# Kernel optimization log

Hardware: AMD Instinct MI355X
Metric: run time of the kernel (lower is better)

Reference implementation:

```python
import jax, jax.numpy as jnp
import numpy as np

B, H, S, D = 2, 16, 2048, 128


def _make_omask(n_heads, seqlen, dtype=jnp.float32):
    # RetNet decay mask: omask[0, h, i, j] = gamma_h^(i-j) for i >= j, else 0
    gamma = 1.0 - 2.0 ** (-5.0 - jnp.arange(n_heads, dtype=jnp.float32))  # [H]
    i = jnp.arange(seqlen)[:, None]
    j = jnp.arange(seqlen)[None, :]
    tri = i >= j                                            # [S, S] lower-triangular incl. diag
    expo = jnp.where(tri, (i - j).astype(jnp.float32), 0.0)  # clamp exponent to avoid overflow
    mask = jnp.where(tri[None], gamma[:, None, None] ** expo[None], 0.0)  # [H, S, S]
    return mask[None].astype(dtype)                          # [1, H, S, S]


def setup_inputs() -> dict:
    key = jax.random.key(0)
    kq, kk, kv = jax.random.split(key, 3)
    q = jax.random.normal(kq, (B, H, S, D), dtype=jnp.float32)
    k = jax.random.normal(kk, (B, H, S, D), dtype=jnp.float32)
    v = jax.random.normal(kv, (B, H, S, D), dtype=jnp.float32)
    omask = _make_omask(H, S)
    return {"q": q, "k": k, "v": v, "omask": omask}


def reference(q, k, v, omask):
    mask = omask[0]                                   # [H, S, S]
    L = jnp.sum(omask, axis=-1, keepdims=True)        # [1, H, S, 1] row sums of decay mask
    qL = q / L                                        # [B, H, S, D]
    # decay-masked retention scores: ((q/L) @ k^T) * D
    scores = jnp.einsum('bhid,bhjd->bhij', qL, k) * mask[None]  # [B, H, S, S]
    # P[b,h,i] = sum_j scores = qL . (mask @ k)  (== einsum with Tbf in original)
    P = jnp.clip(jnp.abs(jnp.sum(scores, axis=-1)), 1.0, None)[..., None]  # [B,H,S,1]
    P = jax.lax.stop_gradient(P)                      # original uses .detach()
    O = jnp.einsum('bhij,bhjd->bhid', scores, v) / P  # [B, H, S, D]
    return O
```

## Files before the change

### kernel.cpp

```cpp
#include <hip/hip_runtime.h>
#include <hip/hip_bf16.h>

namespace {

constexpr int S_DIM = 2048;
constexpr int D_DIM = 128;
constexpr int NH    = 16;
constexpr int QBLK  = 128;
constexpr int KJ    = 32;
constexpr int KROWB = 272;

typedef float  f32x16 __attribute__((ext_vector_type(16)));
typedef __bf16 bf16x8 __attribute__((ext_vector_type(8)));

union U4 { unsigned int w[4]; bf16x8 v; };

__device__ __forceinline__ unsigned int pk2(float a, float b) {
  union { __bf16 h[2]; unsigned int u; } x;
  x.h[0] = (__bf16)a; x.h[1] = (__bf16)b;
  return x.u;
}

__global__ __launch_bounds__(256, 2)
void retnet_fwd(const float* __restrict__ qg, const float* __restrict__ kg,
                const float* __restrict__ vg, float* __restrict__ og) {
  __shared__ __align__(16) unsigned char kbuf[2][KJ * KROWB];

  const int tid  = threadIdx.x;
  const int wave = tid >> 6;
  const int lane = tid & 63;
  const int l31  = lane & 31;
  const int hi   = lane >> 5;

  const int bh = blockIdx.x;
  const int y  = blockIdx.y;
  const int qtile = (y < 8) ? y : (23 - y);
  const int h  = bh & (NH - 1);
  const int qb = qtile * QBLK;

  const float u    = exp2f(-(float)(5 + h));
  const float lng  = log1pf(-u);
  const float lg2g = lng * 1.44269504088896340736f;

  const long long base = (long long)bh * S_DIM * D_DIM;
  const float* qp = qg + base;
  const float* kp = kg + base;
  const float* vp = vg + base;
  float*       op = og + base;

  const int wrow0 = qb + 32 * wave;
  const int ig    = wrow0 + l31;
  const float qscale = -u / expm1f((float)(ig + 1) * lng);

  bf16x8 qf[8];
  {
    const float* qrow = qp + (long long)ig * D_DIM;
    #pragma unroll
    for (int kk = 0; kk < 8; ++kk) {
      const int d0 = 16 * kk + 8 * hi;
      float4 a = *(const float4*)(qrow + d0);
      float4 b = *(const float4*)(qrow + d0 + 4);
      U4 t;
      t.w[0] = pk2(a.x * qscale, a.y * qscale);
      t.w[1] = pk2(a.z * qscale, a.w * qscale);
      t.w[2] = pk2(b.x * qscale, b.y * qscale);
      t.w[3] = pk2(b.z * qscale, b.w * qscale);
      qf[kk] = t.v;
    }
  }

  const float gi1 = exp2f(-lg2g);
  const float gi8 = exp2f(-8.0f * lg2g);
  const float g4[4] = {1.0f, gi1, gi1 * gi1, gi1 * gi1 * gi1};
  const float g8[4] = {1.0f, gi8, gi8 * gi8, gi8 * gi8 * gi8};
  const float gih = hi ? exp2f(-4.0f * lg2g) : 1.0f;

  f32x16 oacc[4] = {};
  float rowsum = 0.0f;

  const int NT     = 4 * qtile + 4;
  const int twlast = 4 * qtile + wave;

  const int sj = tid >> 3;
  const int sd = (tid & 7) * 16;

  float4 ka[4];
  auto loadK = [&](int t) {
    const float* kr = kp + (long long)(KJ * t + sj) * D_DIM + sd;
    #pragma unroll
    for (int c = 0; c < 4; ++c) ka[c] = *(const float4*)(kr + 4 * c);
  };

  auto storeK = [&](int buf) {
    const int s0 = sd >> 3;
    unsigned char* kb = kbuf[buf] + sj * KROWB;
    U4 t;
    t.w[0] = pk2(ka[0].x, ka[0].y); t.w[1] = pk2(ka[0].z, ka[0].w);
    t.w[2] = pk2(ka[1].x, ka[1].y); t.w[3] = pk2(ka[1].z, ka[1].w);
    *(bf16x8*)(kb + (((s0    ) ^ (sj & 15)) * 16)) = t.v;
    t.w[0] = pk2(ka[2].x, ka[2].y); t.w[1] = pk2(ka[2].z, ka[2].w);
    t.w[2] = pk2(ka[3].x, ka[3].y); t.w[3] = pk2(ka[3].z, ka[3].w);
    *(bf16x8*)(kb + (((s0 + 1) ^ (sj & 15)) * 16)) = t.v;
  };

  loadK(0);
  storeK(0);
  __syncthreads();

  for (int t = 0; t < NT; ++t) {
    const int cur = t & 1;
    const bool pre = (t + 1 < NT);
    if (pre) loadK(t + 1);
    __builtin_amdgcn_sched_barrier(0);

    if (t <= twlast) {
      const unsigned char* kb = kbuf[cur];

      f32x16 acc = {};
      #pragma unroll
      for (int kk = 0; kk < 8; ++kk) {
        bf16x8 kf = *(const bf16x8*)(kb + l31 * KROWB + (((2 * kk + hi) ^ (l31 & 15)) * 16));
        acc = __builtin_amdgcn_mfma_f32_32x32x16_bf16(kf, qf[kk], acc, 0, 0, 0);
      }

      const float bb = exp2f((float)(ig - KJ * t) * lg2g) * gih;
      float sv[16];
      if (t == twlast) {
        #pragma unroll
        for (int r = 0; r < 16; ++r) {
          const int jl = (r & 3) + 8 * (r >> 2) + 4 * hi;
          float s = acc[r] * (bb * g8[r >> 2] * g4[r & 3]);
          s = (l31 >= jl) ? s : 0.0f;
          rowsum += s; sv[r] = s;
        }
      } else {
        #pragma unroll
        for (int r = 0; r < 16; ++r) {
          const float s = acc[r] * (bb * g8[r >> 2] * g4[r & 3]);
          rowsum += s; sv[r] = s;
        }
      }

      unsigned int W[4][2], XW[4][2];
      #pragma unroll
      for (int qd = 0; qd < 4; ++qd) {
        W[qd][0] = pk2(sv[4 * qd + 0], sv[4 * qd + 1]);
        W[qd][1] = pk2(sv[4 * qd + 2], sv[4 * qd + 3]);
      }
      #pragma unroll
      for (int qd = 0; qd < 4; ++qd) {
        XW[qd][0] = (unsigned int)__shfl_xor((int)W[qd][0], 32, 64);
        XW[qd][1] = (unsigned int)__shfl_xor((int)W[qd][1], 32, 64);
      }

      #pragma unroll
      for (int jc = 0; jc < 2; ++jc) {
        U4 af;
        if (hi == 0) {
          af.w[0] = W[2 * jc][0];      af.w[1] = W[2 * jc][1];
          af.w[2] = XW[2 * jc][0];     af.w[3] = XW[2 * jc][1];
        } else {
          af.w[0] = XW[2 * jc + 1][0]; af.w[1] = XW[2 * jc + 1][1];
          af.w[2] = W[2 * jc + 1][0];  af.w[3] = W[2 * jc + 1][1];
        }
        const float* vbase =
            vp + (long long)(KJ * t + 16 * jc + 8 * hi) * D_DIM + l31;
        #pragma unroll
        for (int dc = 0; dc < 4; ++dc) {
          const float* vcol = vbase + 32 * dc;
          float ve[8];
          #pragma unroll
          for (int e = 0; e < 8; ++e) ve[e] = vcol[e * D_DIM];
          U4 vf;
          vf.w[0] = pk2(ve[0], ve[1]); vf.w[1] = pk2(ve[2], ve[3]);
          vf.w[2] = pk2(ve[4], ve[5]); vf.w[3] = pk2(ve[6], ve[7]);
          oacc[dc] = __builtin_amdgcn_mfma_f32_32x32x16_bf16(af.v, vf.v, oacc[dc], 0, 0, 0);
        }
      }
    }

    if (pre) storeK(cur ^ 1);
    __syncthreads();
  }

  const float tot  = rowsum + __shfl_xor(rowsum, 32, 64);
  const float invp = 1.0f / fmaxf(fabsf(tot), 1.0f);

  #pragma unroll
  for (int r = 0; r < 16; ++r) {
    const int il = (r & 3) + 8 * (r >> 2) + 4 * hi;
    const float pr = __shfl(invp, il, 32);
    float* orow = op + (long long)(wrow0 + il) * D_DIM + l31;
    #pragma unroll
    for (int dc = 0; dc < 4; ++dc)
      orow[32 * dc] = oacc[dc][r] * pr;
  }
}

}

extern "C" void kernel_launch(void* const* d_in, const int* in_sizes, int n_in,
                              void* d_out, int out_size, void* d_ws, size_t ws_size,
                              hipStream_t stream) {
  const float* q = (const float*)d_in[0];
  const float* k = (const float*)d_in[1];
  const float* v = (const float*)d_in[2];
  float* o = (float*)d_out;
  dim3 grid(32 , 16);
  retnet_fwd<<<grid, 256, 0, stream>>>(q, k, v, o);
}
```

Measured before the change: 506.2 us.

## Precast K to bf16 and transpose V in workspace, split KV across two waves

Two pre-pass kernels convert K to bf16 and write a bf16 transposed copy of V into the workspace. The main kernel then loads its MFMA operands straight from global memory, with no LDS staging, no block-wide syncs and no per-element strided V gathers. The grid is reorganised so each block of two waves owns one 32-row query tile. The waves split the key tiles between them by parity and combine partial outputs and row sums through LDS at the end. This removes repeated fp32-to-bf16 conversion and the uncoalesced V reads, at the cost of extra launches and an extra round trip through workspace memory.

```diff
diff --git a/kernel.cpp b/kernel.cpp
--- a/kernel.cpp
+++ b/kernel.cpp
@@ -6,9 +6,8 @@
 constexpr int S_DIM = 2048;
 constexpr int D_DIM = 128;
 constexpr int NH    = 16;
-constexpr int QBLK  = 128;
-constexpr int KJ    = 32;
-constexpr int KROWB = 272;
+constexpr long long KV_ELEMS = 32LL * S_DIM * D_DIM;
+constexpr size_t    WS_NEED  = (size_t)(2 * KV_ELEMS) * 2;
 
 typedef float  f32x16 __attribute__((ext_vector_type(16)));
 typedef __bf16 bf16x8 __attribute__((ext_vector_type(8)));
@@ -21,10 +20,54 @@
   return x.u;
 }
 
-__global__ __launch_bounds__(256, 2)
-void retnet_fwd(const float* __restrict__ qg, const float* __restrict__ kg,
-                const float* __restrict__ vg, float* __restrict__ og) {
-  __shared__ __align__(16) unsigned char kbuf[2][KJ * KROWB];
+__global__ __launch_bounds__(256)
+void conv_k(const float* __restrict__ k, unsigned short* __restrict__ kw) {
+  const long long i = 8LL * (blockIdx.x * 256 + threadIdx.x);
+  float4 a = *(const float4*)(k + i);
+  float4 b = *(const float4*)(k + i + 4);
+  U4 t;
+  t.w[0] = pk2(a.x, a.y); t.w[1] = pk2(a.z, a.w);
+  t.w[2] = pk2(b.x, b.y); t.w[3] = pk2(b.z, b.w);
+  *(bf16x8*)(kw + i) = t.v;
+}
+
+__global__ __launch_bounds__(256)
+void transp_v(const float* __restrict__ v, unsigned short* __restrict__ vt) {
+  __shared__ float lds[32][33];
+  const int bid = blockIdx.x;
+  const int bh  = bid >> 8;
+  const int rem = bid & 255;
+  const int j0  = (rem >> 2) * 32;
+  const int d0  = (rem & 3) * 32;
+  const int tid = threadIdx.x;
+
+  {
+    const int jl = tid >> 3;
+    const int d4 = (tid & 7) * 4;
+    float4 x = *(const float4*)(v + ((long long)bh * S_DIM + j0 + jl) * D_DIM + d0 + d4);
+    lds[d4 + 0][jl] = x.x; lds[d4 + 1][jl] = x.y;
+    lds[d4 + 2][jl] = x.z; lds[d4 + 3][jl] = x.w;
+  }
+  __syncthreads();
+  {
+    const int dl = tid >> 3;
+    const int j4 = (tid & 7) * 4;
+    const unsigned int w0 = pk2(lds[dl][j4 + 0], lds[dl][j4 + 1]);
+    const unsigned int w1 = pk2(lds[dl][j4 + 2], lds[dl][j4 + 3]);
+    const unsigned long long w = (unsigned long long)w0 | ((unsigned long long)w1 << 32);
+    *(unsigned long long*)(vt + ((long long)bh * D_DIM + d0 + dl) * S_DIM + j0 + j4) = w;
+  }
+}
+
+template <bool PRE>
+__global__ __launch_bounds__(128, 3)
+void retnet_main(const float* __restrict__ qg, const float* __restrict__ kg,
+                 const float* __restrict__ vg,
+                 const unsigned short* __restrict__ kw,
+                 const unsigned short* __restrict__ vtw,
+                 float* __restrict__ og) {
+  __shared__ float xbuf[2][2][64][20];
+  __shared__ float rsbuf[2][32];
 
   const int tid  = threadIdx.x;
   const int wave = tid >> 6;
@@ -32,11 +75,10 @@
   const int l31  = lane & 31;
   const int hi   = lane >> 5;
 
-  const int bh = blockIdx.x;
-  const int y  = blockIdx.y;
-  const int qtile = (y < 8) ? y : (23 - y);
-  const int h  = bh & (NH - 1);
-  const int qb = qtile * QBLK;
+  const int bid = blockIdx.x;
+  const int g   = 63 - (bid >> 5);
+  const int bh  = bid & 31;
+  const int h   = bh & (NH - 1);
 
   const float u    = exp2f(-(float)(5 + h));
   const float lng  = log1pf(-u);
@@ -48,7 +90,7 @@
   const float* vp = vg + base;
   float*       op = og + base;
 
-  const int wrow0 = qb + 32 * wave;
+  const int wrow0 = 32 * g;
   const int ig    = wrow0 + l31;
   const float qscale = -u / expm1f((float)(ig + 1) * lng);
 
@@ -78,93 +120,82 @@
   f32x16 oacc[4] = {};
   float rowsum = 0.0f;
 
-  const int NT     = 4 * qtile + 4;
-  const int twlast = 4 * qtile + wave;
-
-  const int sj = tid >> 3;
-  const int sd = (tid & 7) * 16;
-
-  float4 ka[4];
-  auto loadK = [&](int t) {
-    const float* kr = kp + (long long)(KJ * t + sj) * D_DIM + sd;
-    #pragma unroll
-    for (int c = 0; c < 4; ++c) ka[c] = *(const float4*)(kr + 4 * c);
-  };
-
-  auto storeK = [&](int buf) {
-    const int s0 = sd >> 3;
-    unsigned char* kb = kbuf[buf] + sj * KROWB;
-    U4 t;
-    t.w[0] = pk2(ka[0].x, ka[0].y); t.w[1] = pk2(ka[0].z, ka[0].w);
-    t.w[2] = pk2(ka[1].x, ka[1].y); t.w[3] = pk2(ka[1].z, ka[1].w);
-    *(bf16x8*)(kb + (((s0    ) ^ (sj & 15)) * 16)) = t.v;
-    t.w[0] = pk2(ka[2].x, ka[2].y); t.w[1] = pk2(ka[2].z, ka[2].w);
-    t.w[2] = pk2(ka[3].x, ka[3].y); t.w[3] = pk2(ka[3].z, ka[3].w);
-    *(bf16x8*)(kb + (((s0 + 1) ^ (sj & 15)) * 16)) = t.v;
-  };
-
-  loadK(0);
-  storeK(0);
-  __syncthreads();
-
-  for (int t = 0; t < NT; ++t) {
-    const int cur = t & 1;
-    const bool pre = (t + 1 < NT);
-    if (pre) loadK(t + 1);
-    __builtin_amdgcn_sched_barrier(0);
-
-    if (t <= twlast) {
-      const unsigned char* kb = kbuf[cur];
-
-      f32x16 acc = {};
+  const unsigned short* kwb = kw  + (long long)bh * S_DIM * D_DIM;
+  const unsigned short* vtb = vtw + (long long)bh * D_DIM * S_DIM;
+
+  for (int t = wave; t <= g; t += 2) {
+    const int j0 = 32 * t;
+
+    f32x16 acc = {};
+    if (PRE) {
+      const unsigned short* kb = kwb + (long long)(j0 + l31) * D_DIM + 8 * hi;
       #pragma unroll
       for (int kk = 0; kk < 8; ++kk) {
-        bf16x8 kf = *(const bf16x8*)(kb + l31 * KROWB + (((2 * kk + hi) ^ (l31 & 15)) * 16));
+        bf16x8 kf = *(const bf16x8*)(kb + 16 * kk);
         acc = __builtin_amdgcn_mfma_f32_32x32x16_bf16(kf, qf[kk], acc, 0, 0, 0);
       }
-
-      const float bb = exp2f((float)(ig - KJ * t) * lg2g) * gih;
-      float sv[16];
-      if (t == twlast) {
+    } else {
+      const float* kr = kp + (long long)(j0 + l31) * D_DIM + 8 * hi;
+      #pragma unroll
+      for (int kk = 0; kk < 8; ++kk) {
+        float4 a = *(const float4*)(kr + 16 * kk);
+        float4 b = *(const float4*)(kr + 16 * kk + 4);
+        U4 t;
+        t.w[0] = pk2(a.x, a.y); t.w[1] = pk2(a.z, a.w);
+        t.w[2] = pk2(b.x, b.y); t.w[3] = pk2(b.z, b.w);
+        acc = __builtin_amdgcn_mfma_f32_32x32x16_bf16(t.v, qf[kk], acc, 0, 0, 0);
+      }
+    }
+
+    const float bb = exp2f((float)(ig - j0) * lg2g) * gih;
+    float sv[16];
+    if (t == g) {
+      #pragma unroll
+      for (int r = 0; r < 16; ++r) {
+        const int jl = (r & 3) + 8 * (r >> 2) + 4 * hi;
+        float s = acc[r] * (bb * g8[r >> 2] * g4[r & 3]);
+        s = (l31 >= jl) ? s : 0.0f;
+        rowsum += s; sv[r] = s;
+      }
+    } else {
+      #pragma unroll
+      for (int r = 0; r < 16; ++r) {
+        const float s = acc[r] * (bb * g8[r >> 2] * g4[r & 3]);
+        rowsum += s; sv[r] = s;
+      }
+    }
+
+    unsigned int W[4][2], XW[4][2];
+    #pragma unroll
+    for (int qd = 0; qd < 4; ++qd) {
+      W[qd][0] = pk2(sv[4 * qd + 0], sv[4 * qd + 1]);
+      W[qd][1] = pk2(sv[4 * qd + 2], sv[4 * qd + 3]);
+    }
+    #pragma unroll
+    for (int qd = 0; qd < 4; ++qd) {
+      XW[qd][0] = (unsigned int)__shfl_xor((int)W[qd][0], 32, 64);
+      XW[qd][1] = (unsigned int)__shfl_xor((int)W[qd][1], 32, 64);
+    }
+
+    #pragma unroll
+    for (int jc = 0; jc < 2; ++jc) {
+      U4 af;
+      if (hi == 0) {
+        af.w[0] = W[2 * jc][0];      af.w[1] = W[2 * jc][1];
+        af.w[2] = XW[2 * jc][0];     af.w[3] = XW[2 * jc][1];
+      } else {
+        af.w[0] = XW[2 * jc + 1][0]; af.w[1] = XW[2 * jc + 1][1];
+        af.w[2] = W[2 * jc + 1][0];  af.w[3] = W[2 * jc + 1][1];
+      }
+      if (PRE) {
+        const unsigned short* vrow = vtb + (long long)l31 * S_DIM + (j0 + 16 * jc + 8 * hi);
         #pragma unroll
-        for (int r = 0; r < 16; ++r) {
-          const int jl = (r & 3) + 8 * (r >> 2) + 4 * hi;
-          float s = acc[r] * (bb * g8[r >> 2] * g4[r & 3]);
-          s = (l31 >= jl) ? s : 0.0f;
-          rowsum += s; sv[r] = s;
+        for (int dc = 0; dc < 4; ++dc) {
+          bf16x8 vf = *(const bf16x8*)(vrow + (long long)(32 * dc) * S_DIM);
+          oacc[dc] = __builtin_amdgcn_mfma_f32_32x32x16_bf16(af.v, vf, oacc[dc], 0, 0, 0);
         }
       } else {
-        #pragma unroll
-        for (int r = 0; r < 16; ++r) {
-          const float s = acc[r] * (bb * g8[r >> 2] * g4[r & 3]);
-          rowsum += s; sv[r] = s;
-        }
-      }
-
-      unsigned int W[4][2], XW[4][2];
-      #pragma unroll
-      for (int qd = 0; qd < 4; ++qd) {
-        W[qd][0] = pk2(sv[4 * qd + 0], sv[4 * qd + 1]);
-        W[qd][1] = pk2(sv[4 * qd + 2], sv[4 * qd + 3]);
-      }
-      #pragma unroll
-      for (int qd = 0; qd < 4; ++qd) {
-        XW[qd][0] = (unsigned int)__shfl_xor((int)W[qd][0], 32, 64);
-        XW[qd][1] = (unsigned int)__shfl_xor((int)W[qd][1], 32, 64);
-      }
-
-      #pragma unroll
-      for (int jc = 0; jc < 2; ++jc) {
-        U4 af;
-        if (hi == 0) {
-          af.w[0] = W[2 * jc][0];      af.w[1] = W[2 * jc][1];
-          af.w[2] = XW[2 * jc][0];     af.w[3] = XW[2 * jc][1];
-        } else {
-          af.w[0] = XW[2 * jc + 1][0]; af.w[1] = XW[2 * jc + 1][1];
-          af.w[2] = W[2 * jc + 1][0];  af.w[3] = W[2 * jc + 1][1];
-        }
-        const float* vbase =
-            vp + (long long)(KJ * t + 16 * jc + 8 * hi) * D_DIM + l31;
+        const float* vbase = vp + (long long)(j0 + 16 * jc + 8 * hi) * D_DIM + l31;
         #pragma unroll
         for (int dc = 0; dc < 4; ++dc) {
           const float* vcol = vbase + 32 * dc;
@@ -178,12 +209,37 @@
         }
       }
     }
-
-    if (pre) storeK(cur ^ 1);
-    __syncthreads();
-  }
-
-  const float tot  = rowsum + __shfl_xor(rowsum, 32, 64);
+  }
+
+  const int sendf = wave ? 0 : 2;
+  #pragma unroll
+  for (int f = 0; f < 2; ++f) {
+    const f32x16 src = oacc[sendf + f];
+    #pragma unroll
+    for (int m = 0; m < 4; ++m) {
+      float4 tmp;
+      tmp.x = src[4 * m + 0]; tmp.y = src[4 * m + 1];
+      tmp.z = src[4 * m + 2]; tmp.w = src[4 * m + 3];
+      *(float4*)(&xbuf[wave][f][lane][4 * m]) = tmp;
+    }
+  }
+  const float rtot = rowsum + __shfl_xor(rowsum, 32, 64);
+  if (hi == 0) rsbuf[wave][l31] = rtot;
+  __syncthreads();
+
+  const int keepf = wave ? 2 : 0;
+  #pragma unroll
+  for (int f = 0; f < 2; ++f) {
+    #pragma unroll
+    for (int m = 0; m < 4; ++m) {
+      float4 x = *(const float4*)(&xbuf[wave ^ 1][f][lane][4 * m]);
+      oacc[keepf + f][4 * m + 0] += x.x;
+      oacc[keepf + f][4 * m + 1] += x.y;
+      oacc[keepf + f][4 * m + 2] += x.z;
+      oacc[keepf + f][4 * m + 3] += x.w;
+    }
+  }
+  const float tot  = rtot + rsbuf[wave ^ 1][l31];
   const float invp = 1.0f / fmaxf(fabsf(tot), 1.0f);
 
   #pragma unroll
@@ -192,8 +248,10 @@
     const float pr = __shfl(invp, il, 32);
     float* orow = op + (long long)(wrow0 + il) * D_DIM + l31;
     #pragma unroll
-    for (int dc = 0; dc < 4; ++dc)
+    for (int f = 0; f < 2; ++f) {
+      const int dc = keepf + f;
       orow[32 * dc] = oacc[dc][r] * pr;
+    }
   }
 }
 
@@ -206,6 +264,14 @@
   const float* k = (const float*)d_in[1];
   const float* v = (const float*)d_in[2];
   float* o = (float*)d_out;
-  dim3 grid(32 , 16);
-  retnet_fwd<<<grid, 256, 0, stream>>>(q, k, v, o);
-}
+
+  if (ws_size >= WS_NEED) {
+    unsigned short* kw = (unsigned short*)d_ws;
+    unsigned short* vt = kw + KV_ELEMS;
+    conv_k  <<<(int)(KV_ELEMS / 8 / 256), 256, 0, stream>>>(k, kw);
+    transp_v<<<32 * 64 * 4,               256, 0, stream>>>(v, vt);
+    retnet_main<true ><<<2048, 128, 0, stream>>>(q, k, v, kw, vt, o);
+  } else {
+    retnet_main<false><<<2048, 128, 0, stream>>>(q, k, v, nullptr, nullptr, o);
+  }
+}
```

After: 521.7 us. 1.03x slower.
